# Optimization experiments

Measured on AMD Instinct MI355X. Metric: run time of the kernel, lower is better.

The kernel has to match this reference:

```python
import jax, jax.numpy as jnp
import numpy as np

B, N, M, C, H = 256, 4096, 64, 512, 4
IN, OUT = 64, 64
EPS = 1e-8

def setup_inputs():
    key = jax.random.key(0)
    ks = jax.random.split(key, 8)
    def w(k, shape, scale=0.05):
        return jax.random.normal(k, shape, dtype=jnp.float32) * scale
    return {
        "in_data": jax.random.normal(ks[0], (B, IN), dtype=jnp.float32),
        "memory": jax.random.normal(ks[1], (B, N, M), dtype=jnp.float32),
        "h0": jnp.zeros((B, C), jnp.float32),
        "c0": jnp.zeros((B, C), jnp.float32),
        "prev_weights": jnp.zeros((2 * H, B, N), jnp.float32),
        "prev_reads": jax.random.normal(ks[2], (H, B, M), dtype=jnp.float32),
        "W_ih": w(ks[3], (4 * C, IN + H * M)),
        "b_ih": jnp.zeros((4 * C,), jnp.float32),
        "W_hh": w(ks[4], (4 * C, C)),
        "b_hh": jnp.zeros((4 * C,), jnp.float32),
        "W_out": w(ks[5], (OUT, C + H * M)),
        "b_out": jnp.zeros((OUT,), jnp.float32),
        "W_addr": w(ks[6], (2 * H, M + 6, C)),
        "b_addr": jnp.zeros((2 * H, M + 6), jnp.float32),
        "W_ea": w(ks[7], (H, 2 * M, C)),
        "b_ea": jnp.zeros((H, 2 * M), jnp.float32),
    }


def reference(in_data, memory, h0, c0, prev_weights, prev_reads,
              W_ih, b_ih, W_hh, b_hh, W_out, b_out,
              W_addr, b_addr, W_ea, b_ea):
    # ---- controller: LSTMCell over [input, prev_reads...] ----
    x = jnp.concatenate([in_data] + [prev_reads[i] for i in range(H)], axis=-1)  # [B, IN+H*M]
    gates = x @ W_ih.T + b_ih + h0 @ W_hh.T + b_hh                               # [B, 4C]
    i_g, f_g, g_g, o_g = jnp.split(gates, 4, axis=-1)
    c = jax.nn.sigmoid(f_g) * c0 + jax.nn.sigmoid(i_g) * jnp.tanh(g_g)
    h = jax.nn.sigmoid(o_g) * jnp.tanh(c)

    # ---- heads: alternate read / write, sequential over memory ----
    mem = memory
    reads = []
    for hi in range(2 * H):
        p = c @ W_addr[hi].T + b_addr[hi]                     # [B, M+6]
        k = jnp.tanh(p[:, :M])                                # key
        beta = jax.nn.softplus(p[:, M:M + 1])                 # key strength
        gate = jax.nn.sigmoid(p[:, M + 1:M + 2])              # interpolation gate
        s = jax.nn.softmax(p[:, M + 2:M + 5], axis=-1)        # shift weights (3)
        gamma = 1.0 + jax.nn.softplus(p[:, M + 5:M + 6])      # sharpening
        # content addressing: cosine similarity against all memory rows
        dot = jnp.einsum('bnm,bm->bn', mem, k)                # [B, N]
        norms = jnp.linalg.norm(mem, axis=-1) * jnp.linalg.norm(k, axis=-1, keepdims=True)
        wc = jax.nn.softmax(beta * dot / (norms + EPS), axis=-1)
        # interpolation with previous weights
        wg = gate * wc + (1.0 - gate) * prev_weights[hi]
        # circular shift convolution (shifts -1, 0, +1)
        ws = (s[:, 0:1] * jnp.roll(wg, 1, axis=-1)
              + s[:, 1:2] * wg
              + s[:, 2:3] * jnp.roll(wg, -1, axis=-1))
        # sharpening
        wp = ws ** gamma
        w = wp / (jnp.sum(wp, axis=-1, keepdims=True) + EPS)
        if hi % 2 == 0:  # read head
            reads.append(jnp.einsum('bn,bnm->bm', w, mem))
        else:            # write head: erase then add
            ea = c @ W_ea[hi // 2].T + b_ea[hi // 2]          # [B, 2M]
            e = jax.nn.sigmoid(ea[:, :M])
            a = jnp.tanh(ea[:, M:])
            mem = mem * (1.0 - w[:, :, None] * e[:, None, :]) + w[:, :, None] * a[:, None, :]

    # ---- output layer over [h, reads...] ----
    state = jnp.concatenate([h] + reads, axis=-1)             # [B, C+H*M]
    return jax.nn.sigmoid(state @ W_out.T + b_out)            # [B, OUT]
```

## Files before the change

kernel.cpp:

```cpp
#include <hip/hip_runtime.h>
#include <hip/hip_fp16.h>
#include <math.h>

#define EPSF 1e-8f
#define NN 4096
#define BB 256
#define PH ((size_t)BB * NN)

__device__ __forceinline__ float sigf(float x) { return 1.0f / (1.0f + expf(-x)); }
__device__ __forceinline__ float softplusf(float x) { return x > 20.0f ? x : log1pf(expf(x)); }
__device__ __forceinline__ float dot4(float4 a, float4 b) {
  return a.x * b.x + a.y * b.y + a.z * b.z + a.w * b.w;
}
__device__ __forceinline__ unsigned short f2bf(float x) {
  unsigned int u = __float_as_uint(x);
  unsigned int r = (u + 0x7FFF + ((u >> 16) & 1)) >> 16;
  return (unsigned short)r;
}
__device__ __forceinline__ float bf2f(unsigned int lo16) {
  return __uint_as_float(lo16 << 16);
}

__device__ __forceinline__ float gather_x(const float* __restrict__ in_data,
                                          const float* __restrict__ prev_reads,
                                          const float* __restrict__ h0,
                                          int row, int k) {
  if (k < 64) return in_data[row * 64 + k];
  if (k < 320) { int i = (k - 64) >> 6, m = (k - 64) & 63; return prev_reads[((size_t)i * 256 + row) * 64 + m]; }
  return h0[row * 512 + (k - 320)];
}

__global__ __launch_bounds__(256) void gemm_gates_kernel(
    const float* __restrict__ in_data, const float* __restrict__ prev_reads,
    const float* __restrict__ h0, const float* __restrict__ W_ih,
    const float* __restrict__ W_hh, const float* __restrict__ b_ih,
    const float* __restrict__ b_hh, float* __restrict__ gates) {
  __shared__ float As[16][33];
  __shared__ float Ws[16][65];
  int tid = threadIdx.x, tx = tid & 15, ty = tid >> 4;
  int row0 = blockIdx.y * 32, col0 = blockIdx.x * 64;
  float acc[2][4] = {{0,0,0,0},{0,0,0,0}};
  for (int k0 = 0; k0 < 832; k0 += 16) {
    const float* Wp; int kw, KW;
    if (k0 < 320) { Wp = W_ih; kw = k0; KW = 320; }
    else          { Wp = W_hh; kw = k0 - 320; KW = 512; }
    for (int i = tid; i < 32 * 16; i += 256) {
      int rr = i >> 4, cc = i & 15;
      As[cc][rr] = gather_x(in_data, prev_reads, h0, row0 + rr, k0 + cc);
    }
    for (int i = tid; i < 64 * 16; i += 256) {
      int rr = i >> 4, cc = i & 15;
      Ws[cc][rr] = Wp[(size_t)(col0 + rr) * KW + kw + cc];
    }
    __syncthreads();
#pragma unroll
    for (int kk = 0; kk < 16; kk++) {
      float a0 = As[kk][ty * 2 + 0], a1 = As[kk][ty * 2 + 1];
      float w0 = Ws[kk][tx * 4 + 0], w1 = Ws[kk][tx * 4 + 1];
      float w2 = Ws[kk][tx * 4 + 2], w3 = Ws[kk][tx * 4 + 3];
      acc[0][0] += a0 * w0; acc[0][1] += a0 * w1; acc[0][2] += a0 * w2; acc[0][3] += a0 * w3;
      acc[1][0] += a1 * w0; acc[1][1] += a1 * w1; acc[1][2] += a1 * w2; acc[1][3] += a1 * w3;
    }
    __syncthreads();
  }
  for (int i = 0; i < 2; i++)
    for (int j = 0; j < 4; j++) {
      int cc = col0 + tx * 4 + j;
      gates[(size_t)(row0 + ty * 2 + i) * 2048 + cc] = acc[i][j] + b_ih[cc] + b_hh[cc];
    }
}

__global__ void lstm_elem_kernel(const float* __restrict__ gates,
                                 const float* __restrict__ c0,
                                 float* __restrict__ c, float* __restrict__ h) {
  int idx = blockIdx.x * 256 + threadIdx.x;
  if (idx >= 256 * 512) return;
  int b = idx >> 9, u = idx & 511;
  const float* g = gates + (size_t)b * 2048;
  float ig = sigf(g[u]), fg = sigf(g[512 + u]);
  float gg = tanhf(g[1024 + u]), og = sigf(g[1536 + u]);
  float cv = fg * c0[idx] + ig * gg;
  c[idx] = cv;
  h[idx] = og * tanhf(cv);
}

__global__ __launch_bounds__(256) void gemm_heads_kernel(
    const float* __restrict__ C, const float* __restrict__ W_addr,
    const float* __restrict__ W_ea, const float* __restrict__ b_addr,
    const float* __restrict__ b_ea, float* __restrict__ p_raw) {
  __shared__ float As[16][33];
  __shared__ float Ws[16][65];
  int tid = threadIdx.x, tx = tid & 15, ty = tid >> 4;
  int row0 = blockIdx.y * 32, col0 = blockIdx.x * 64;
  float acc[2][4] = {{0,0,0,0},{0,0,0,0}};
  for (int k0 = 0; k0 < 512; k0 += 16) {
    for (int i = tid; i < 32 * 16; i += 256) {
      int rr = i >> 4, cc = i & 15;
      As[cc][rr] = C[(size_t)(row0 + rr) * 512 + k0 + cc];
    }
    for (int i = tid; i < 64 * 16; i += 256) {
      int rr = i >> 4, cc = i & 15;
      int col = col0 + rr;
      float v = 0.f;
      if (col < 560) v = W_addr[(size_t)col * 512 + k0 + cc];
      else if (col < 1072) v = W_ea[(size_t)(col - 560) * 512 + k0 + cc];
      Ws[cc][rr] = v;
    }
    __syncthreads();
#pragma unroll
    for (int kk = 0; kk < 16; kk++) {
      float a0 = As[kk][ty * 2 + 0], a1 = As[kk][ty * 2 + 1];
      float w0 = Ws[kk][tx * 4 + 0], w1 = Ws[kk][tx * 4 + 1];
      float w2 = Ws[kk][tx * 4 + 2], w3 = Ws[kk][tx * 4 + 3];
      acc[0][0] += a0 * w0; acc[0][1] += a0 * w1; acc[0][2] += a0 * w2; acc[0][3] += a0 * w3;
      acc[1][0] += a1 * w0; acc[1][1] += a1 * w1; acc[1][2] += a1 * w2; acc[1][3] += a1 * w3;
    }
    __syncthreads();
  }
  for (int i = 0; i < 2; i++)
    for (int j = 0; j < 4; j++) {
      int col = col0 + tx * 4 + j;
      if (col < 1072) {
        float bias = col < 560 ? b_addr[col] : b_ea[col - 560];
        p_raw[(size_t)(row0 + ty * 2 + i) * 1072 + col] = acc[i][j] + bias;
      }
    }
}

__global__ void params_kernel(const float* __restrict__ p_raw,
    float* __restrict__ knorm, float* __restrict__ betav,
    float* __restrict__ gatev, float* __restrict__ sv,
    float* __restrict__ gammav, float* __restrict__ combo,
    float* __restrict__ scal) {
  int b = blockIdx.x, m = threadIdx.x;
  const float* p = p_raw + (size_t)b * 1072;
  float kv[7];
#pragma unroll
  for (int hi = 0; hi < 7; hi++) {
    float k = tanhf(p[hi * 70 + m]);
    kv[hi] = k;
    float s = k * k;
#pragma unroll
    for (int d = 1; d < 64; d <<= 1) s += __shfl_xor(s, d);
    if (m == 0) {
      int hb = hi * BB + b;
      knorm[hb] = sqrtf(s);
      betav[hb] = softplusf(p[hi * 70 + 64]);
      gatev[hb] = sigf(p[hi * 70 + 65]);
      float a0 = p[hi * 70 + 66], a1 = p[hi * 70 + 67], a2 = p[hi * 70 + 68];
      float mm = fmaxf(a0, fmaxf(a1, a2));
      float e0 = expf(a0 - mm), e1 = expf(a1 - mm), e2 = expf(a2 - mm);
      float es = e0 + e1 + e2;
      sv[hb * 3 + 0] = e0 / es; sv[hb * 3 + 1] = e1 / es; sv[hb * 3 + 2] = e2 / es;
      gammav[hb] = 1.0f + softplusf(p[hi * 70 + 69]);
    }
  }
  float e1 = sigf(p[560 + 0 * 128 + m]),  a1v = tanhf(p[560 + 0 * 128 + 64 + m]);
  float e3 = sigf(p[560 + 1 * 128 + m]),  a3v = tanhf(p[560 + 1 * 128 + 64 + m]);
  float e5 = sigf(p[560 + 2 * 128 + m]),  a5v = tanhf(p[560 + 2 * 128 + 64 + m]);
  size_t bm = (size_t)b * 64 + m;
  combo[0 * 16384 + bm] = kv[0];  combo[1 * 16384 + bm] = kv[1];
  combo[2 * 16384 + bm] = kv[2];  combo[3 * 16384 + bm] = e1 * kv[2];
  combo[4 * 16384 + bm] = kv[3];  combo[5 * 16384 + bm] = e1 * kv[3];
  combo[6 * 16384 + bm] = a1v;    combo[7 * 16384 + bm] = e1 * a1v;
  combo[8 * 16384 + bm] = e1;     combo[9 * 16384 + bm] = e1 * e1;
  combo[10 * 16384 + bm] = kv[4]; combo[11 * 16384 + bm] = kv[5];
  combo[12 * 16384 + bm] = kv[6]; combo[13 * 16384 + bm] = e5 * kv[6];
  combo[14 * 16384 + bm] = a5v;   combo[15 * 16384 + bm] = e5 * a5v;
  combo[16 * 16384 + bm] = e5;    combo[17 * 16384 + bm] = e5 * e5;
  combo[18 * 16384 + bm] = e3;    combo[19 * 16384 + bm] = a3v;
  float s0 = a1v * kv[2], s1 = a1v * kv[3], s2 = a1v * a1v, s3 = a5v * kv[6], s4 = a5v * a5v;
#pragma unroll
  for (int d = 1; d < 64; d <<= 1) {
    s0 += __shfl_xor(s0, d); s1 += __shfl_xor(s1, d); s2 += __shfl_xor(s2, d);
    s3 += __shfl_xor(s3, d); s4 += __shfl_xor(s4, d);
  }
  if (m == 0) {
    scal[b * 8 + 0] = s0; scal[b * 8 + 1] = s1; scal[b * 8 + 2] = s2;
    scal[b * 8 + 3] = s3; scal[b * 8 + 4] = s4;
  }
}

#define CL(j, q) (*(const float4*)(cb + (j) * 64 + (q) * 4))

__global__ __launch_bounds__(256) void phase1_kernel(
    const float* __restrict__ mem, const float* __restrict__ combo,
    const float* __restrict__ scal, const float* __restrict__ knorm,
    const float* __restrict__ betav, unsigned short* __restrict__ mem_bf,
    __half* __restrict__ P) {
  __shared__ float cb[640];
  int b = blockIdx.y, tid = threadIdx.x;
  for (int i = tid; i < 640; i += 256)
    cb[i] = combo[(size_t)(i >> 6) * 16384 + b * 64 + (i & 63)];
  __syncthreads();
  float kn0 = knorm[b], be0 = betav[b];
  float kn1 = knorm[BB + b], be1 = betav[BB + b];
  float cak2 = scal[b * 8 + 0], cak3 = scal[b * 8 + 1], caa1 = scal[b * 8 + 2];
  int n = blockIdx.x * 256 + tid;
  size_t bo = (size_t)b * NN;
  const float4* rp = (const float4*)mem + (bo + n) * 16;
  ushort4* op = (ushort4*)mem_bf + (bo + n) * 16;
  float a[11];
#pragma unroll
  for (int k = 0; k < 11; k++) a[k] = 0.f;
#pragma unroll
  for (int q = 0; q < 16; q++) {
    float4 v = rp[q];
    ushort4 o;
    o.x = f2bf(v.x); o.y = f2bf(v.y); o.z = f2bf(v.z); o.w = f2bf(v.w);
    op[q] = o;
    float4 sq = make_float4(v.x * v.x, v.y * v.y, v.z * v.z, v.w * v.w);
    a[0] += dot4(v, CL(0, q)); a[1] += dot4(v, CL(1, q));
    a[2] += dot4(v, CL(2, q)); a[3] += dot4(v, CL(3, q));
    a[4] += dot4(v, CL(4, q)); a[5] += dot4(v, CL(5, q));
    a[6] += dot4(v, CL(6, q)); a[7] += dot4(v, CL(7, q));
    a[8] += sq.x + sq.y + sq.z + sq.w;
    a[9] += dot4(sq, CL(8, q)); a[10] += dot4(sq, CL(9, q));
  }
  float rn = sqrtf(a[8]);
  P[0 * PH + bo + n] = __float2half(be0 * a[0] / (rn * kn0 + EPSF));
  P[1 * PH + bo + n] = __float2half(be1 * a[1] / (rn * kn1 + EPSF));
  P[2 * PH + bo + n] = __float2half(a[2]);
  P[3 * PH + bo + n] = __float2half(a[3] - cak2);
  P[4 * PH + bo + n] = __float2half(a[4]);
  P[5 * PH + bo + n] = __float2half(a[5] - cak3);
  P[6 * PH + bo + n] = __float2half(a[8]);
  P[7 * PH + bo + n] = __float2half(a[9] - a[6]);
  P[8 * PH + bo + n] = __float2half(a[10] - 2.f * a[7] + caa1);
}

__global__ __launch_bounds__(512) void chain_kernel(
    const __half* __restrict__ P, __half* __restrict__ w_g,
    const float* __restrict__ knorm, const float* __restrict__ betav,
    const float* __restrict__ gatev, const float* __restrict__ sv,
    const float* __restrict__ gammav, const float* __restrict__ prev_w,
    int group) {
  __shared__ float wg[NN];
  __shared__ float red[24];
  int b = blockIdx.x, hy = blockIdx.y, tid = threadIdx.x;
  int lane = tid & 63, wv = tid >> 6;
  int head, u_head = 0;
  const __half *SC = nullptr, *Da = nullptr, *Dbc = nullptr;
  const __half *S0p = nullptr, *T1p = nullptr, *T2p = nullptr;
  if (group == 0)      { head = hy;     SC = P + (size_t)hy * PH; }
  else if (group == 1) { head = 2 + hy; Da = P + (size_t)(2 + 2 * hy) * PH; Dbc = P + (size_t)(3 + 2 * hy) * PH;
                         S0p = P + 6 * PH; T1p = P + 7 * PH; T2p = P + 8 * PH; u_head = 1; }
  else if (group == 2) { head = 4 + hy; SC = P + (size_t)hy * PH; }
  else                 { head = 6;      Da = P + 2 * PH; Dbc = P + 3 * PH;
                         S0p = P + 4 * PH; T1p = P + 5 * PH; T2p = P + 6 * PH; u_head = 5; }
  int hb = head * BB + b;
  float kn = knorm[hb], be = betav[hb], ga = gatev[hb], gm = gammav[hb];
  float s0 = sv[hb * 3 + 0], s1 = sv[hb * 3 + 1], s2 = sv[hb * 3 + 2];
  size_t bo = (size_t)b * NN;
  const float* pw = prev_w + (size_t)head * PH + bo;
  const __half* ug = w_g + ((size_t)u_head * BB + b) * NN;
  __half* wout = w_g + ((size_t)head * BB + b) * NN;
  float sc[8];
  float mx = -1e30f;
#pragma unroll
  for (int i = 0; i < 8; i++) {
    int n = tid + i * 512;
    float scv;
    if (SC != nullptr) {
      scv = __half2float(SC[bo + n]);
    } else {
      float u = __half2float(ug[n]);
      float d = __half2float(Da[bo + n]) - u * __half2float(Dbc[bo + n]);
      float nn2 = __half2float(S0p[bo + n]) - 2.f * u * __half2float(T1p[bo + n])
                + u * u * __half2float(T2p[bo + n]);
      nn2 = fmaxf(nn2, 0.f);
      scv = be * d / (sqrtf(nn2) * kn + EPSF);
    }
    sc[i] = scv; mx = fmaxf(mx, scv);
  }
#pragma unroll
  for (int m = 1; m < 64; m <<= 1) mx = fmaxf(mx, __shfl_xor(mx, m));
  if (lane == 0) red[wv] = mx;
  __syncthreads();
  mx = red[0];
#pragma unroll
  for (int w = 1; w < 8; w++) mx = fmaxf(mx, red[w]);
  float sum = 0.f;
#pragma unroll
  for (int i = 0; i < 8; i++) { sc[i] = expf(sc[i] - mx); sum += sc[i]; }
#pragma unroll
  for (int m = 1; m < 64; m <<= 1) sum += __shfl_xor(sum, m);
  if (lane == 0) red[8 + wv] = sum;
  __syncthreads();
  sum = 0.f;
#pragma unroll
  for (int w = 0; w < 8; w++) sum += red[8 + w];
  float inv = 1.0f / sum;
#pragma unroll
  for (int i = 0; i < 8; i++) {
    int n = tid + i * 512;
    wg[n] = ga * (sc[i] * inv) + (1.f - ga) * pw[n];
  }
  __syncthreads();
  float wp[8];
  float sum2 = 0.f;
#pragma unroll
  for (int i = 0; i < 8; i++) {
    int n = tid + i * 512;
    float wsv = s0 * wg[(n + NN - 1) & (NN - 1)] + s1 * wg[n] + s2 * wg[(n + 1) & (NN - 1)];
    wp[i] = powf(wsv, gm);
    sum2 += wp[i];
  }
#pragma unroll
  for (int m = 1; m < 64; m <<= 1) sum2 += __shfl_xor(sum2, m);
  if (lane == 0) red[16 + wv] = sum2;
  __syncthreads();
  sum2 = 0.f;
#pragma unroll
  for (int w = 0; w < 8; w++) sum2 += red[16 + w];
  float invs = 1.0f / (sum2 + EPSF);
#pragma unroll
  for (int i = 0; i < 8; i++) {
    int n = tid + i * 512;
    wout[n] = __float2half(wp[i] * invs);
  }
}

__global__ __launch_bounds__(256) void phase2_kernel(
    const unsigned short* __restrict__ mem_bf, const float* __restrict__ combo,
    const float* __restrict__ scal, const float* __restrict__ knorm,
    const float* __restrict__ betav, const __half* __restrict__ w_g,
    __half* __restrict__ P) {
  __shared__ float cb[1280];
  int b = blockIdx.y, tid = threadIdx.x;
  for (int i = tid; i < 1280; i += 256)
    cb[i] = combo[(size_t)(i >> 6) * 16384 + b * 64 + (i & 63)];
  __syncthreads();
  float kn4 = knorm[4 * BB + b], be4 = betav[4 * BB + b];
  float kn5 = knorm[5 * BB + b], be5 = betav[5 * BB + b];
  float cak6 = scal[b * 8 + 3], caa5 = scal[b * 8 + 4];
  int n = blockIdx.x * 256 + tid;
  size_t bo = (size_t)b * NN;
  const uint4* mb = (const uint4*)mem_bf + (bo + n) * 8;
  float u1 = __half2float(w_g[((size_t)1 * BB + b) * NN + n]);
  float u3 = __half2float(w_g[((size_t)3 * BB + b) * NN + n]);
  float t[9];
#pragma unroll
  for (int k = 0; k < 9; k++) t[k] = 0.f;
#pragma unroll
  for (int g = 0; g < 8; g++) {
    uint4 uv = mb[g];
#pragma unroll
    for (int h = 0; h < 2; h++) {
      unsigned int pa = h ? uv.z : uv.x;
      unsigned int pb = h ? uv.w : uv.y;
      float4 v;
      v.x = bf2f(pa & 0xFFFFu); v.y = bf2f(pa >> 16);
      v.z = bf2f(pb & 0xFFFFu); v.w = bf2f(pb >> 16);
      int q = g * 2 + h;
      float4 e1v = CL(8, q), a1v = CL(6, q), e3v = CL(18, q), a3v = CL(19, q);
      float4 m1, m2;
      m1.x = v.x * (1.f - u1 * e1v.x) + u1 * a1v.x;
      m1.y = v.y * (1.f - u1 * e1v.y) + u1 * a1v.y;
      m1.z = v.z * (1.f - u1 * e1v.z) + u1 * a1v.z;
      m1.w = v.w * (1.f - u1 * e1v.w) + u1 * a1v.w;
      m2.x = m1.x * (1.f - u3 * e3v.x) + u3 * a3v.x;
      m2.y = m1.y * (1.f - u3 * e3v.y) + u3 * a3v.y;
      m2.z = m1.z * (1.f - u3 * e3v.z) + u3 * a3v.z;
      m2.w = m1.w * (1.f - u3 * e3v.w) + u3 * a3v.w;
      float4 sq = make_float4(m2.x * m2.x, m2.y * m2.y, m2.z * m2.z, m2.w * m2.w);
      t[0] += dot4(m2, CL(10, q)); t[1] += dot4(m2, CL(11, q));
      t[2] += dot4(m2, CL(12, q)); t[3] += dot4(m2, CL(13, q));
      t[4] += dot4(m2, CL(14, q)); t[5] += dot4(m2, CL(15, q));
      t[6] += sq.x + sq.y + sq.z + sq.w;
      t[7] += dot4(sq, CL(16, q)); t[8] += dot4(sq, CL(17, q));
    }
  }
  float rn = sqrtf(t[6]);
  P[0 * PH + bo + n] = __float2half(be4 * t[0] / (rn * kn4 + EPSF));
  P[1 * PH + bo + n] = __float2half(be5 * t[1] / (rn * kn5 + EPSF));
  P[2 * PH + bo + n] = __float2half(t[2]);
  P[3 * PH + bo + n] = __float2half(t[3] - cak6);
  P[4 * PH + bo + n] = __float2half(t[6]);
  P[5 * PH + bo + n] = __float2half(t[7] - t[4]);
  P[6 * PH + bo + n] = __float2half(t[8] - 2.f * t[5] + caa5);
}

__global__ __launch_bounds__(256) void phase3_kernel(
    const unsigned short* __restrict__ mem_bf, const float* __restrict__ combo,
    const __half* __restrict__ w_g, float* __restrict__ reads) {
  __shared__ float cb[1280];
  __shared__ __half ws[7 * 512];
  __shared__ float sred[4 * 4 * 16 * 4];
  int b = blockIdx.y, chunk = blockIdx.x, tid = threadIdx.x;
  for (int i = tid; i < 1280; i += 256)
    cb[i] = combo[(size_t)(i >> 6) * 16384 + b * 64 + (i & 63)];
  int nbase = chunk * 512;
  for (int i = tid; i < 7 * 512; i += 256) {
    int hh = i >> 9, nn = i & 511;
    ws[i] = w_g[((size_t)hh * BB + b) * NN + nbase + nn];
  }
  __syncthreads();
  int wv = tid >> 6, lane = tid & 63, q = lane & 15, rl = lane >> 4;
  float4 e1v = CL(8, q), a1v = CL(6, q), e3v = CL(18, q), a3v = CL(19, q);
  float4 e5v = CL(16, q), a5v = CL(14, q);
  size_t bo = (size_t)b * NN;
  const ushort4* mbr = (const ushort4*)mem_bf + bo * 16;
  float A[4][4];
#pragma unroll
  for (int j = 0; j < 4; j++)
#pragma unroll
    for (int cmp = 0; cmp < 4; cmp++) A[j][cmp] = 0.f;
#pragma unroll 4
  for (int t = 0; t < 32; t++) {
    int nl = t * 16 + wv * 4 + rl;
    int n = nbase + nl;
    ushort4 uv = mbr[(size_t)n * 16 + q];
    float vx = bf2f(uv.x), vy = bf2f(uv.y), vz = bf2f(uv.z), vw = bf2f(uv.w);
    float w0v = __half2float(ws[0 * 512 + nl]);
    float u1  = __half2float(ws[1 * 512 + nl]);
    float w2v = __half2float(ws[2 * 512 + nl]);
    float u3  = __half2float(ws[3 * 512 + nl]);
    float w4v = __half2float(ws[4 * 512 + nl]);
    float u5  = __half2float(ws[5 * 512 + nl]);
    float w6v = __half2float(ws[6 * 512 + nl]);
    A[0][0] += w0v * vx; A[0][1] += w0v * vy; A[0][2] += w0v * vz; A[0][3] += w0v * vw;
    float m1x = vx * (1.f - u1 * e1v.x) + u1 * a1v.x;
    float m1y = vy * (1.f - u1 * e1v.y) + u1 * a1v.y;
    float m1z = vz * (1.f - u1 * e1v.z) + u1 * a1v.z;
    float m1w = vw * (1.f - u1 * e1v.w) + u1 * a1v.w;
    A[1][0] += w2v * m1x; A[1][1] += w2v * m1y; A[1][2] += w2v * m1z; A[1][3] += w2v * m1w;
    float m2x = m1x * (1.f - u3 * e3v.x) + u3 * a3v.x;
    float m2y = m1y * (1.f - u3 * e3v.y) + u3 * a3v.y;
    float m2z = m1z * (1.f - u3 * e3v.z) + u3 * a3v.z;
    float m2w = m1w * (1.f - u3 * e3v.w) + u3 * a3v.w;
    A[2][0] += w4v * m2x; A[2][1] += w4v * m2y; A[2][2] += w4v * m2z; A[2][3] += w4v * m2w;
    float m3x = m2x * (1.f - u5 * e5v.x) + u5 * a5v.x;
    float m3y = m2y * (1.f - u5 * e5v.y) + u5 * a5v.y;
    float m3z = m2z * (1.f - u5 * e5v.z) + u5 * a5v.z;
    float m3w = m2w * (1.f - u5 * e5v.w) + u5 * a5v.w;
    A[3][0] += w6v * m3x; A[3][1] += w6v * m3y; A[3][2] += w6v * m3z; A[3][3] += w6v * m3w;
  }
#pragma unroll
  for (int j = 0; j < 4; j++)
#pragma unroll
    for (int cmp = 0; cmp < 4; cmp++) {
      float x = A[j][cmp];
      x += __shfl_xor(x, 16);
      x += __shfl_xor(x, 32);
      A[j][cmp] = x;
    }
  if (rl == 0)
#pragma unroll
    for (int j = 0; j < 4; j++)
#pragma unroll
      for (int cmp = 0; cmp < 4; cmp++)
        sred[((j * 4 + wv) * 16 + q) * 4 + cmp] = A[j][cmp];
  __syncthreads();
  if (tid < 256) {
    int j = tid >> 6, qq = (tid >> 2) & 15, cc = tid & 3;
    float s = 0.f;
#pragma unroll
    for (int w = 0; w < 4; w++) s += sred[((j * 4 + w) * 16 + qq) * 4 + cc];
    atomicAdd(&reads[(size_t)j * 16384 + b * 64 + qq * 4 + cc], s);
  }
}

__global__ __launch_bounds__(256) void gemm_out_kernel(
    const float* __restrict__ h, const float* __restrict__ reads,
    const float* __restrict__ W_out, const float* __restrict__ b_out,
    float* __restrict__ out) {
  __shared__ float As[16][33];
  __shared__ float Ws[16][65];
  int tid = threadIdx.x, tx = tid & 15, ty = tid >> 4;
  int row0 = blockIdx.y * 32;
  float acc[2][4] = {{0,0,0,0},{0,0,0,0}};
  for (int k0 = 0; k0 < 768; k0 += 16) {
    for (int i = tid; i < 32 * 16; i += 256) {
      int rr = i >> 4, cc = i & 15;
      int row = row0 + rr, k = k0 + cc;
      float v;
      if (k < 512) v = h[row * 512 + k];
      else { int slot = (k - 512) >> 6, m = (k - 512) & 63; v = reads[((size_t)slot * 256 + row) * 64 + m]; }
      As[cc][rr] = v;
    }
    for (int i = tid; i < 64 * 16; i += 256) {
      int rr = i >> 4, cc = i & 15;
      Ws[cc][rr] = W_out[(size_t)rr * 768 + k0 + cc];
    }
    __syncthreads();
#pragma unroll
    for (int kk = 0; kk < 16; kk++) {
      float a0 = As[kk][ty * 2 + 0], a1 = As[kk][ty * 2 + 1];
      float w0 = Ws[kk][tx * 4 + 0], w1 = Ws[kk][tx * 4 + 1];
      float w2 = Ws[kk][tx * 4 + 2], w3 = Ws[kk][tx * 4 + 3];
      acc[0][0] += a0 * w0; acc[0][1] += a0 * w1; acc[0][2] += a0 * w2; acc[0][3] += a0 * w3;
      acc[1][0] += a1 * w0; acc[1][1] += a1 * w1; acc[1][2] += a1 * w2; acc[1][3] += a1 * w3;
    }
    __syncthreads();
  }
  for (int i = 0; i < 2; i++)
    for (int j = 0; j < 4; j++) {
      int cc = tx * 4 + j;
      out[(size_t)(row0 + ty * 2 + i) * 64 + cc] = sigf(acc[i][j] + b_out[cc]);
    }
}

extern "C" void kernel_launch(void* const* d_in, const int* in_sizes, int n_in,
                              void* d_out, int out_size, void* d_ws, size_t ws_size,
                              hipStream_t stream) {
  const float* in_data = (const float*)d_in[0];
  const float* memory  = (const float*)d_in[1];
  const float* h0      = (const float*)d_in[2];
  const float* c0      = (const float*)d_in[3];
  const float* prev_w  = (const float*)d_in[4];
  const float* prev_r  = (const float*)d_in[5];
  const float* W_ih    = (const float*)d_in[6];
  const float* b_ih    = (const float*)d_in[7];
  const float* W_hh    = (const float*)d_in[8];
  const float* b_hh    = (const float*)d_in[9];
  const float* W_out   = (const float*)d_in[10];
  const float* b_out   = (const float*)d_in[11];
  const float* W_addr  = (const float*)d_in[12];
  const float* b_addr  = (const float*)d_in[13];
  const float* W_ea    = (const float*)d_in[14];
  const float* b_ea    = (const float*)d_in[15];
  float* out = (float*)d_out;
  (void)in_sizes; (void)n_in; (void)out_size; (void)ws_size;

  float* ws = (float*)d_ws;
  size_t off = 0;
  auto alloc = [&](size_t n) { float* p = ws + off; off += (n + 63) & ~(size_t)63; return p; };
  float* gates  = alloc(256 * 2048);
  float* cbuf   = alloc(256 * 512);
  float* hbuf   = alloc(256 * 512);
  float* p_raw  = alloc(256 * 1072);
  float* knorm  = alloc(8 * 256);
  float* betav  = alloc(8 * 256);
  float* gatev  = alloc(8 * 256);
  float* sv     = alloc(8 * 256 * 3);
  float* gammav = alloc(8 * 256);
  float* combo  = alloc(20 * 16384);
  float* scal   = alloc(256 * 8);
  __half* P     = (__half*)alloc(9 * PH / 2);
  float* reads  = alloc(4 * 16384);
  unsigned short* mem_bf = (unsigned short*)alloc(33554432);
  __half* w_g   = (__half*)alloc(7 * BB * NN / 2);

  gemm_gates_kernel<<<dim3(32, 8), 256, 0, stream>>>(in_data, prev_r, h0, W_ih, W_hh, b_ih, b_hh, gates);
  lstm_elem_kernel<<<(256 * 512 + 255) / 256, 256, 0, stream>>>(gates, c0, cbuf, hbuf);
  gemm_heads_kernel<<<dim3(17, 8), 256, 0, stream>>>(cbuf, W_addr, W_ea, b_addr, b_ea, p_raw);
  params_kernel<<<256, 64, 0, stream>>>(p_raw, knorm, betav, gatev, sv, gammav, combo, scal);
  hipMemsetAsync(reads, 0, 4 * 16384 * sizeof(float), stream);

  phase1_kernel<<<dim3(16, 256), 256, 0, stream>>>(memory, combo, scal, knorm, betav, mem_bf, P);
  chain_kernel<<<dim3(256, 2), 512, 0, stream>>>(P, w_g, knorm, betav, gatev, sv, gammav, prev_w, 0);
  chain_kernel<<<dim3(256, 2), 512, 0, stream>>>(P, w_g, knorm, betav, gatev, sv, gammav, prev_w, 1);
  phase2_kernel<<<dim3(16, 256), 256, 0, stream>>>(mem_bf, combo, scal, knorm, betav, w_g, P);
  chain_kernel<<<dim3(256, 2), 512, 0, stream>>>(P, w_g, knorm, betav, gatev, sv, gammav, prev_w, 2);
  chain_kernel<<<dim3(256, 1), 512, 0, stream>>>(P, w_g, knorm, betav, gatev, sv, gammav, prev_w, 3);
  phase3_kernel<<<dim3(8, 256), 256, 0, stream>>>(mem_bf, combo, w_g, reads);

  gemm_out_kernel<<<dim3(1, 8), 256, 0, stream>>>(hbuf, reads, W_out, b_out, out);
}
```

Before: 968.0 us.

## Stage memory rows through swizzled LDS for coalesced loads in phase1/phase2

In phase1 and phase2, each thread used to read one full 256-byte memory row by itself, so accesses across a wavefront were strided. The kernels now load a 128-row tile cooperatively with coalesced float4/uint4 loads into XOR-swizzled shared memory, and the bf16 copy is written coalesced as well. Two threads then split each row's dot products and combine them with a shuffle, and the grid doubles to cover the smaller tiles. This costs extra LDS per block, a barrier and a shuffle reduction, and may lower occupancy.

New measurement: 888.1 us. 1.09x faster.

```diff
diff --git a/kernel.cpp b/kernel.cpp
--- a/kernel.cpp
+++ b/kernel.cpp
@@ -189,26 +189,36 @@
     const float* __restrict__ betav, unsigned short* __restrict__ mem_bf,
     __half* __restrict__ P) {
   __shared__ float cb[640];
+  __shared__ float4 tile[128 * 16];
   int b = blockIdx.y, tid = threadIdx.x;
   for (int i = tid; i < 640; i += 256)
     cb[i] = combo[(size_t)(i >> 6) * 16384 + b * 64 + (i & 63)];
+  int n0 = blockIdx.x * 128;
+  size_t bo = (size_t)b * NN;
+  const float4* src = (const float4*)mem + (bo + n0) * 16;
+  ushort4* dst = (ushort4*)mem_bf + (bo + n0) * 16;
+#pragma unroll
+  for (int i = 0; i < 8; i++) {
+    int idx = tid + i * 256;
+    float4 v = src[idx];
+    int r = idx >> 4, q = idx & 15;
+    tile[r * 16 + (q ^ (r & 15))] = v;
+    ushort4 o;
+    o.x = f2bf(v.x); o.y = f2bf(v.y); o.z = f2bf(v.z); o.w = f2bf(v.w);
+    dst[idx] = o;
+  }
   __syncthreads();
   float kn0 = knorm[b], be0 = betav[b];
   float kn1 = knorm[BB + b], be1 = betav[BB + b];
   float cak2 = scal[b * 8 + 0], cak3 = scal[b * 8 + 1], caa1 = scal[b * 8 + 2];
-  int n = blockIdx.x * 256 + tid;
-  size_t bo = (size_t)b * NN;
-  const float4* rp = (const float4*)mem + (bo + n) * 16;
-  ushort4* op = (ushort4*)mem_bf + (bo + n) * 16;
+  int row = tid >> 1, half = tid & 1;
   float a[11];
 #pragma unroll
   for (int k = 0; k < 11; k++) a[k] = 0.f;
 #pragma unroll
-  for (int q = 0; q < 16; q++) {
-    float4 v = rp[q];
-    ushort4 o;
-    o.x = f2bf(v.x); o.y = f2bf(v.y); o.z = f2bf(v.z); o.w = f2bf(v.w);
-    op[q] = o;
+  for (int j = 0; j < 8; j++) {
+    int q = half * 8 + j;
+    float4 v = tile[row * 16 + (q ^ (row & 15))];
     float4 sq = make_float4(v.x * v.x, v.y * v.y, v.z * v.z, v.w * v.w);
     a[0] += dot4(v, CL(0, q)); a[1] += dot4(v, CL(1, q));
     a[2] += dot4(v, CL(2, q)); a[3] += dot4(v, CL(3, q));
@@ -217,16 +227,21 @@
     a[8] += sq.x + sq.y + sq.z + sq.w;
     a[9] += dot4(sq, CL(8, q)); a[10] += dot4(sq, CL(9, q));
   }
-  float rn = sqrtf(a[8]);
-  P[0 * PH + bo + n] = __float2half(be0 * a[0] / (rn * kn0 + EPSF));
-  P[1 * PH + bo + n] = __float2half(be1 * a[1] / (rn * kn1 + EPSF));
-  P[2 * PH + bo + n] = __float2half(a[2]);
-  P[3 * PH + bo + n] = __float2half(a[3] - cak2);
-  P[4 * PH + bo + n] = __float2half(a[4]);
-  P[5 * PH + bo + n] = __float2half(a[5] - cak3);
-  P[6 * PH + bo + n] = __float2half(a[8]);
-  P[7 * PH + bo + n] = __float2half(a[9] - a[6]);
-  P[8 * PH + bo + n] = __float2half(a[10] - 2.f * a[7] + caa1);
+#pragma unroll
+  for (int k = 0; k < 11; k++) a[k] += __shfl_xor(a[k], 1);
+  if (half == 0) {
+    int n = n0 + row;
+    float rn = sqrtf(a[8]);
+    P[0 * PH + bo + n] = __float2half(be0 * a[0] / (rn * kn0 + EPSF));
+    P[1 * PH + bo + n] = __float2half(be1 * a[1] / (rn * kn1 + EPSF));
+    P[2 * PH + bo + n] = __float2half(a[2]);
+    P[3 * PH + bo + n] = __float2half(a[3] - cak2);
+    P[4 * PH + bo + n] = __float2half(a[4]);
+    P[5 * PH + bo + n] = __float2half(a[5] - cak3);
+    P[6 * PH + bo + n] = __float2half(a[8]);
+    P[7 * PH + bo + n] = __float2half(a[9] - a[6]);
+    P[8 * PH + bo + n] = __float2half(a[10] - 2.f * a[7] + caa1);
+  }
 }
 
 __global__ __launch_bounds__(512) void chain_kernel(
@@ -327,24 +342,35 @@
     const float* __restrict__ betav, const __half* __restrict__ w_g,
     __half* __restrict__ P) {
   __shared__ float cb[1280];
+  __shared__ uint4 tileb[128 * 8];
   int b = blockIdx.y, tid = threadIdx.x;
   for (int i = tid; i < 1280; i += 256)
     cb[i] = combo[(size_t)(i >> 6) * 16384 + b * 64 + (i & 63)];
+  int n0 = blockIdx.x * 128;
+  size_t bo = (size_t)b * NN;
+  const uint4* src = (const uint4*)mem_bf + (bo + n0) * 8;
+#pragma unroll
+  for (int i = 0; i < 4; i++) {
+    int idx = tid + i * 256;
+    uint4 u = src[idx];
+    int r = idx >> 3, g = idx & 7;
+    tileb[r * 8 + (g ^ (r & 7))] = u;
+  }
   __syncthreads();
   float kn4 = knorm[4 * BB + b], be4 = betav[4 * BB + b];
   float kn5 = knorm[5 * BB + b], be5 = betav[5 * BB + b];
   float cak6 = scal[b * 8 + 3], caa5 = scal[b * 8 + 4];
-  int n = blockIdx.x * 256 + tid;
-  size_t bo = (size_t)b * NN;
-  const uint4* mb = (const uint4*)mem_bf + (bo + n) * 8;
+  int row = tid >> 1, half = tid & 1;
+  int n = n0 + row;
   float u1 = __half2float(w_g[((size_t)1 * BB + b) * NN + n]);
   float u3 = __half2float(w_g[((size_t)3 * BB + b) * NN + n]);
   float t[9];
 #pragma unroll
   for (int k = 0; k < 9; k++) t[k] = 0.f;
 #pragma unroll
-  for (int g = 0; g < 8; g++) {
-    uint4 uv = mb[g];
+  for (int j = 0; j < 4; j++) {
+    int g = half * 4 + j;
+    uint4 uv = tileb[row * 8 + (g ^ (row & 7))];
 #pragma unroll
     for (int h = 0; h < 2; h++) {
       unsigned int pa = h ? uv.z : uv.x;
@@ -371,14 +397,18 @@
       t[7] += dot4(sq, CL(16, q)); t[8] += dot4(sq, CL(17, q));
     }
   }
-  float rn = sqrtf(t[6]);
-  P[0 * PH + bo + n] = __float2half(be4 * t[0] / (rn * kn4 + EPSF));
-  P[1 * PH + bo + n] = __float2half(be5 * t[1] / (rn * kn5 + EPSF));
-  P[2 * PH + bo + n] = __float2half(t[2]);
-  P[3 * PH + bo + n] = __float2half(t[3] - cak6);
-  P[4 * PH + bo + n] = __float2half(t[6]);
-  P[5 * PH + bo + n] = __float2half(t[7] - t[4]);
-  P[6 * PH + bo + n] = __float2half(t[8] - 2.f * t[5] + caa5);
+#pragma unroll
+  for (int k = 0; k < 9; k++) t[k] += __shfl_xor(t[k], 1);
+  if (half == 0) {
+    float rn = sqrtf(t[6]);
+    P[0 * PH + bo + n] = __float2half(be4 * t[0] / (rn * kn4 + EPSF));
+    P[1 * PH + bo + n] = __float2half(be5 * t[1] / (rn * kn5 + EPSF));
+    P[2 * PH + bo + n] = __float2half(t[2]);
+    P[3 * PH + bo + n] = __float2half(t[3] - cak6);
+    P[4 * PH + bo + n] = __float2half(t[6]);
+    P[5 * PH + bo + n] = __float2half(t[7] - t[4]);
+    P[6 * PH + bo + n] = __float2half(t[8] - 2.f * t[5] + caa5);
+  }
 }
 
 __global__ __launch_bounds__(256) void phase3_kernel(
@@ -548,10 +578,10 @@
   params_kernel<<<256, 64, 0, stream>>>(p_raw, knorm, betav, gatev, sv, gammav, combo, scal);
   hipMemsetAsync(reads, 0, 4 * 16384 * sizeof(float), stream);
 
-  phase1_kernel<<<dim3(16, 256), 256, 0, stream>>>(memory, combo, scal, knorm, betav, mem_bf, P);
+  phase1_kernel<<<dim3(32, 256), 256, 0, stream>>>(memory, combo, scal, knorm, betav, mem_bf, P);
   chain_kernel<<<dim3(256, 2), 512, 0, stream>>>(P, w_g, knorm, betav, gatev, sv, gammav, prev_w, 0);
   chain_kernel<<<dim3(256, 2), 512, 0, stream>>>(P, w_g, knorm, betav, gatev, sv, gammav, prev_w, 1);
-  phase2_kernel<<<dim3(16, 256), 256, 0, stream>>>(mem_bf, combo, scal, knorm, betav, w_g, P);
+  phase2_kernel<<<dim3(32, 256), 256, 0, stream>>>(mem_bf, combo, scal, knorm, betav, w_g, P);
   chain_kernel<<<dim3(256, 2), 512, 0, stream>>>(P, w_g, knorm, betav, gatev, sv, gammav, prev_w, 2);
   chain_kernel<<<dim3(256, 1), 512, 0, stream>>>(P, w_g, knorm, betav, gatev, sv, gammav, prev_w, 3);
   phase3_kernel<<<dim3(8, 256), 256, 0, stream>>>(mem_bf, combo, w_g, reads);
```
